# Kernel optimization log

Measured on AMD Instinct MI355X. Metric: run time of the kernel, lower is better.

Reference implementation:

```python
import jax, jax.numpy as jnp
import numpy as np

N = 100000
E = 3200000
D = 64


def setup_inputs() -> dict:
    key = jax.random.key(0)
    k1, k2, k3 = jax.random.split(key, 3)
    indices = jax.random.randint(k1, (2, E), 0, N, dtype=jnp.int64) if jax.config.jax_enable_x64 else jax.random.randint(k1, (2, E), 0, N, dtype=jnp.int32)
    values = jax.random.uniform(k2, (E,), dtype=jnp.float32)
    b = jax.random.normal(k3, (N, D), dtype=jnp.float32)
    return {"indices": indices, "values": values, "shape": N, "b": b}


def reference(indices, values, shape, b):
    # sparse COO [N,N] @ dense [N,D]:
    # out[r] = sum over edges e with row[e]==r of values[e] * b[col[e]]
    row, col = indices[0], indices[1]
    msgs = values[:, None] * b[col]            # [E, D] gather + scale
    out = jax.ops.segment_sum(msgs, row, num_segments=shape)  # [N, D] scatter-add
    return out
```

## Files before the change

### kernel.cpp

```cpp
#include <hip/hip_runtime.h>
#include <hip/hip_bf16.h>


#define D 64
#define BROWS 64
#define MAXNB 2048
#define CAP 2560
#define NM (CAP / 256)
#define SPILLCAP 8192

#define CROWS 2048
#define NCB 64
#define SCH_A 2048
#define CBLK 4352
#define NBLK_C 16
#define CAPC (CBLK * NBLK_C)

#define SCH 4096

__global__ __launch_bounds__(256) void spmm_atomic_kernel(
    const int* __restrict__ rows, const int* __restrict__ cols,
    const float* __restrict__ vals, const float* __restrict__ b,
    float* __restrict__ out, int E) {
  long long gid = (long long)blockIdx.x * blockDim.x + threadIdx.x;
  int e = (int)(gid >> 6);
  int d = (int)(gid & 63);
  if (e >= E) return;
  atomicAdd(&out[(long long)rows[e] * D + d], vals[e] * b[(long long)cols[e] * D + d]);
}

__device__ __forceinline__ unsigned bf16rne(float x) {
  unsigned u = __float_as_uint(x);
  return (u + 0x7FFFu + ((u >> 16) & 1u)) >> 16;
}
__global__ __launch_bounds__(256) void convert_kernel(
    const float4* __restrict__ src, uint2* __restrict__ dst, int n4) {
  int i = blockIdx.x * 256 + threadIdx.x;
  if (i >= n4) return;
  float4 f = src[i];
  dst[i] = make_uint2(bf16rne(f.x) | (bf16rne(f.y) << 16),
                      bf16rne(f.z) | (bf16rne(f.w) << 16));
}

__global__ __launch_bounds__(256) void coarse_scatter_kernel(
    const int* __restrict__ rows, const int* __restrict__ cols,
    const float* __restrict__ vals, int* __restrict__ gcoarse,
    uint2* __restrict__ cslab_lo, uint2* __restrict__ cslab_hi, int csplit,
    uint4* __restrict__ spill, int* __restrict__ spill_cnt, int E) {
  __shared__ uint2 stage[SCH_A];
  __shared__ unsigned char sbin[SCH_A];
  __shared__ int h[NCB];
  __shared__ int lst[NCB];
  __shared__ int gb[NCB];
  int t = threadIdx.x;
  if (t < NCB) h[t] = 0;
  __syncthreads();
  int start = blockIdx.x * SCH_A;
  int ec = E - start;
  if (ec > SCH_A) ec = SCH_A;

  int bin[8];
  int rank[8];
  unsigned key[8];
  float vv[8];
#pragma unroll
  for (int ki = 0; ki < 2; ki++) {
    int e0 = start + ki * 1024 + t * 4;
    int j0 = ki * 4;
    if (e0 + 3 < E) {
      int4 r = ((const int4*)(rows + start + ki * 1024))[t];
      int4 c = ((const int4*)(cols + start + ki * 1024))[t];
      float4 v = ((const float4*)(vals + start + ki * 1024))[t];
      int rl[4] = {r.x, r.y, r.z, r.w};
      int cl[4] = {c.x, c.y, c.z, c.w};
      float vl[4] = {v.x, v.y, v.z, v.w};
#pragma unroll
      for (int j = 0; j < 4; j++) {
        int bn = rl[j] >> 11;
        bin[j0 + j] = bn;
        rank[j0 + j] = atomicAdd(&h[bn], 1);
        key[j0 + j] = ((unsigned)(rl[j] & (CROWS - 1)) << 17) | (unsigned)cl[j];
        vv[j0 + j] = vl[j];
      }
    } else {
#pragma unroll
      for (int j = 0; j < 4; j++) {
        int e = e0 + j;
        bin[j0 + j] = -1;
        if (e < E) {
          int r = rows[e];
          int bn = r >> 11;
          bin[j0 + j] = bn;
          rank[j0 + j] = atomicAdd(&h[bn], 1);
          key[j0 + j] = ((unsigned)(r & (CROWS - 1)) << 17) | (unsigned)cols[e];
          vv[j0 + j] = vals[e];
        }
      }
    }
  }
  __syncthreads();
  if (t < NCB) {
    int c = h[t];
    int x = c;
#pragma unroll
    for (int off = 1; off < 64; off <<= 1) {
      int u = __shfl_up(x, off);
      if (t >= off) x += u;
    }
    lst[t] = x - c;
    gb[t] = c ? atomicAdd(&gcoarse[t], c) : 0;
  }
  __syncthreads();
#pragma unroll
  for (int j = 0; j < 8; j++) {
    if (bin[j] >= 0) {
      int pos = lst[bin[j]] + rank[j];
      stage[pos] = make_uint2(key[j], __float_as_uint(vv[j]));
      sbin[pos] = (unsigned char)bin[j];
    }
  }
  __syncthreads();
  for (int i = t; i < ec; i += 256) {
    int bn = sbin[i];
    uint2 p = stage[i];
    int pin = gb[bn] + (i - lst[bn]);
    if (pin < CAPC) {
      uint2* slab = (bn < csplit) ? (cslab_lo + (size_t)bn * CAPC)
                                  : (cslab_hi + (size_t)(bn - csplit) * CAPC);
      slab[pin] = p;
    } else {
      int sp = atomicAdd(spill_cnt, 1);
      if (sp < SPILLCAP)
        spill[sp] = make_uint4((unsigned)((bn << 11) | (int)(p.x >> 17)),
                               p.x & 0x1FFFFu, p.y, 0u);
    }
  }
}

__global__ __launch_bounds__(256) void fine_scatter_kernel(
    const int* __restrict__ gcoarse, const uint2* __restrict__ cslab_lo,
    const uint2* __restrict__ cslab_hi, int csplit, int* __restrict__ gcount,
    uint2* __restrict__ pairs, uint4* __restrict__ spill,
    int* __restrict__ spill_cnt) {
  int c = blockIdx.x >> 4;
  int blk = blockIdx.x & 15;
  int cnt = gcoarse[c];
  if (cnt > CAPC) cnt = CAPC;
  int base = blk * CBLK;
  int ec = cnt - base;
  if (ec <= 0) return;
  if (ec > CBLK) ec = CBLK;
  const uint2* src = ((c < csplit) ? (cslab_lo + (size_t)c * CAPC)
                                   : (cslab_hi + (size_t)(c - csplit) * CAPC)) +
                     base;
  __shared__ uint2 stage[CBLK];
  __shared__ unsigned char sbin[CBLK];
  __shared__ int h[32];
  __shared__ int lst[32];
  __shared__ int gb[32];
  int t = threadIdx.x;
  if (t < 32) h[t] = 0;
  __syncthreads();
  int rank[17];
#pragma unroll
  for (int k = 0; k < 17; k++) {
    int i = k * 256 + t;
    if (i < ec) rank[k] = atomicAdd(&h[src[i].x >> 23], 1);
  }
  __syncthreads();
  if (t < 32) {
    int cn = h[t];
    int x = cn;
#pragma unroll
    for (int off = 1; off < 32; off <<= 1) {
      int u = __shfl_up(x, off);
      if (t >= off) x += u;
    }
    lst[t] = x - cn;
    gb[t] = cn ? atomicAdd(&gcount[c * 32 + t], cn) : 0;
  }
  __syncthreads();
#pragma unroll
  for (int k = 0; k < 17; k++) {
    int i = k * 256 + t;
    if (i < ec) {
      uint2 p = src[i];
      int f = (int)(p.x >> 23);
      int pos = lst[f] + rank[k];
      unsigned key2 = (((p.x >> 17) & 63u) << 26) | ((p.x & 0x1FFFFu) << 7);
      stage[pos] = make_uint2(key2, p.y);
      sbin[pos] = (unsigned char)f;
    }
  }
  __syncthreads();
  for (int i = t; i < ec; i += 256) {
    int f = sbin[i];
    uint2 p = stage[i];
    int pin = gb[f] + (i - lst[f]);
    int gbkt = c * 32 + f;
    if (pin < CAP) {
      pairs[(size_t)gbkt * CAP + pin] = p;
    } else {
      int sp = atomicAdd(spill_cnt, 1);
      if (sp < SPILLCAP)
        spill[sp] = make_uint4((unsigned)(gbkt * 64 + (int)(p.x >> 26)),
                               (p.x >> 7) & 0x1FFFFu, p.y, 0u);
    }
  }
}

__global__ __launch_bounds__(256) void binned_scatter_kernel(
    const int* __restrict__ rows, const int* __restrict__ cols,
    const float* __restrict__ vals, int* __restrict__ gcount,
    uint2* __restrict__ pairs, uint4* __restrict__ spill,
    int* __restrict__ spill_cnt, int E, int NB) {
  __shared__ int h[MAXNB];
  __shared__ int baseoff[MAXNB];
  int t = threadIdx.x;
  for (int i = t; i < NB; i += 256) h[i] = 0;
  __syncthreads();
  int start = blockIdx.x * SCH;
  bool full = (start + SCH <= E);
  int4 r4[4];
  int rank[16];
  if (full) {
#pragma unroll
    for (int ki = 0; ki < 4; ki++) {
      r4[ki] = ((const int4*)(rows + start + ki * 1024))[t];
      rank[4 * ki + 0] = atomicAdd(&h[r4[ki].x >> 6], 1);
      rank[4 * ki + 1] = atomicAdd(&h[r4[ki].y >> 6], 1);
      rank[4 * ki + 2] = atomicAdd(&h[r4[ki].z >> 6], 1);
      rank[4 * ki + 3] = atomicAdd(&h[r4[ki].w >> 6], 1);
    }
  } else {
#pragma unroll
    for (int ki = 0; ki < 4; ki++) {
      int e = start + ki * 1024 + t * 4;
      int4 rr = make_int4(0, 0, 0, 0);
      if (e + 0 < E) { rr.x = rows[e + 0]; rank[4 * ki + 0] = atomicAdd(&h[rr.x >> 6], 1); }
      if (e + 1 < E) { rr.y = rows[e + 1]; rank[4 * ki + 1] = atomicAdd(&h[rr.y >> 6], 1); }
      if (e + 2 < E) { rr.z = rows[e + 2]; rank[4 * ki + 2] = atomicAdd(&h[rr.z >> 6], 1); }
      if (e + 3 < E) { rr.w = rows[e + 3]; rank[4 * ki + 3] = atomicAdd(&h[rr.w >> 6], 1); }
      r4[ki] = rr;
    }
  }
  __syncthreads();
  for (int i = t; i < NB; i += 256)
    baseoff[i] = h[i] ? atomicAdd(&gcount[i], h[i]) : 0;
  __syncthreads();
#pragma unroll
  for (int ki = 0; ki < 4; ki++) {
    int e = start + ki * 1024 + t * 4;
    int cc[4], rr[4] = {r4[ki].x, r4[ki].y, r4[ki].z, r4[ki].w};
    float vv[4];
    if (full) {
      int4 c4 = ((const int4*)(cols + start + ki * 1024))[t];
      float4 v4 = ((const float4*)(vals + start + ki * 1024))[t];
      cc[0] = c4.x; cc[1] = c4.y; cc[2] = c4.z; cc[3] = c4.w;
      vv[0] = v4.x; vv[1] = v4.y; vv[2] = v4.z; vv[3] = v4.w;
    } else {
#pragma unroll
      for (int j = 0; j < 4; j++) {
        cc[j] = (e + j < E) ? cols[e + j] : 0;
        vv[j] = (e + j < E) ? vals[e + j] : 0.f;
      }
    }
#pragma unroll
    for (int j = 0; j < 4; j++) {
      if (e + j < E) {
        int r = rr[j];
        int bk = r >> 6;
        int pin = baseoff[bk] + rank[4 * ki + j];
        if (pin < CAP) {
          unsigned key = ((unsigned)(r & (BROWS - 1)) << 26) |
                         ((unsigned)cc[j] << 7);
          pairs[(size_t)bk * CAP + pin] = make_uint2(key, __float_as_uint(vv[j]));
        } else {
          int sp = atomicAdd(spill_cnt, 1);
          if (sp < SPILLCAP)
            spill[sp] = make_uint4((unsigned)r, (unsigned)cc[j],
                                   __float_as_uint(vv[j]), 0u);
        }
      }
    }
  }
}

__global__ __launch_bounds__(256) void spmm_fused_kernel(
    const uint2* __restrict__ pairs, const int* __restrict__ gcount,
    const uint2* __restrict__ b16, float* __restrict__ out, int N) {
  __shared__ uint2 lp[CAP];
  __shared__ int cnt64[64];
  __shared__ int roff[65];
  int bkt = blockIdx.x;
  int cnt = gcount[bkt];
  if (cnt > CAP) cnt = CAP;
  const uint2* src = pairs + (size_t)bkt * CAP;
  int t = threadIdx.x;
  if (t < 64) cnt64[t] = 0;
  __syncthreads();
  uint2 mine[NM];
  int rk[NM];
#pragma unroll
  for (int k = 0; k < NM; k++) {
    int i = t + k * 256;
    if (i < cnt) {
      mine[k] = src[i];
      rk[k] = atomicAdd(&cnt64[mine[k].x >> 26], 1);
    }
  }
  __syncthreads();
  if (t < 64) {
    int v = cnt64[t];
    int x = v;
    for (int off = 1; off < 64; off <<= 1) {
      int u = __shfl_up(x, off);
      if (t >= off) x += u;
    }
    roff[t] = x - v;
    if (t == 63) roff[64] = x;
  }
  __syncthreads();
#pragma unroll
  for (int k = 0; k < NM; k++) {
    int i = t + k * 256;
    if (i < cnt)
      lp[roff[mine[k].x >> 26] + rk[k]] =
          make_uint2(mine[k].x & 0x03FFFF80u, mine[k].y);
  }
  __syncthreads();
  int lane = t & 63;
  int wv = t >> 6;
  int g = lane >> 3;
  int l8 = lane & 7;
  int gid32 = wv * 8 + g;
  const char* bq = (const char*)b16 + (l8 << 4);
  int row_base = bkt * BROWS;
#pragma unroll
  for (int rr = 0; rr < 2; rr++) {
    int r = gid32 + 32 * rr;
    int gr = row_base + r;
    int j0 = roff[r], j1 = roff[r + 1];
    float acc[8] = {0.f, 0.f, 0.f, 0.f, 0.f, 0.f, 0.f, 0.f};
    for (int base = j0; base < j1; base += 4) {
      uint4 bv[4];
      float vv[4];
#pragma unroll
      for (int k = 0; k < 4; k++) {
        int idx = base + k;
        int ic = (idx < j1) ? idx : j0;
        uint2 p = lp[ic];
        bv[k] = *(const uint4*)(bq + p.x);
        vv[k] = (idx < j1) ? __uint_as_float(p.y) : 0.f;
      }
#pragma unroll
      for (int k = 0; k < 4; k++) {
        unsigned u0 = bv[k].x, u1 = bv[k].y, u2 = bv[k].z, u3 = bv[k].w;
        float v = vv[k];
        acc[0] += v * __uint_as_float(u0 << 16);
        acc[1] += v * __uint_as_float(u0 & 0xFFFF0000u);
        acc[2] += v * __uint_as_float(u1 << 16);
        acc[3] += v * __uint_as_float(u1 & 0xFFFF0000u);
        acc[4] += v * __uint_as_float(u2 << 16);
        acc[5] += v * __uint_as_float(u2 & 0xFFFF0000u);
        acc[6] += v * __uint_as_float(u3 << 16);
        acc[7] += v * __uint_as_float(u3 & 0xFFFF0000u);
      }
    }
    if (gr < N) {
      float4* dst = (float4*)(out + (size_t)gr * D + l8 * 8);
      dst[0] = make_float4(acc[0], acc[1], acc[2], acc[3]);
      dst[1] = make_float4(acc[4], acc[5], acc[6], acc[7]);
    }
  }
}

__global__ __launch_bounds__(256) void spill_fix_kernel(
    const uint4* __restrict__ spill, const int* __restrict__ spill_cnt,
    const float* __restrict__ b, float* __restrict__ out) {
  int n = *spill_cnt;
  if (n > SPILLCAP) n = SPILLCAP;
  int lane = threadIdx.x & 63;
  int w = (int)((blockIdx.x * blockDim.x + threadIdx.x) >> 6);
  int nw = (int)((gridDim.x * blockDim.x) >> 6);
  for (int s = w; s < n; s += nw) {
    uint4 e = spill[s];
    atomicAdd(&out[(size_t)e.x * D + lane],
              __uint_as_float(e.z) * b[(size_t)e.y * D + lane]);
  }
}

extern "C" void kernel_launch(void* const* d_in, const int* in_sizes, int n_in,
                              void* d_out, int out_size, void* d_ws, size_t ws_size,
                              hipStream_t stream) {
  const int* indices = (const int*)d_in[0];
  const float* vals  = (const float*)d_in[1];
  const float* b     = (const float*)d_in[3];

  int E = in_sizes[1];
  int N = in_sizes[3] / D;
  const int* rows = indices;
  const int* cols = indices + E;

  int NB = (N + BROWS - 1) / BROWS;
  int NC = (N + CROWS - 1) / CROWS;
  int n4 = N * D / 4;

  size_t off_gcount  = 0;
  size_t off_gcoarse = off_gcount + (size_t)MAXNB * 4;
  size_t off_scnt    = off_gcoarse + (size_t)NCB * 4;
  size_t off_spill   = (off_scnt + 4 + 15) & ~(size_t)15;
  size_t off_pairs   = off_spill + (size_t)SPILLCAP * 16;
  size_t npbkt       = (size_t)NC * 32;
  size_t off_b16     = off_pairs + npbkt * CAP * 8;
  size_t off_cextra  = off_b16 + (size_t)N * D * 2;
  size_t outbytes    = (size_t)out_size * 4;
  int csplit = (int)(outbytes / ((size_t)CAPC * 8));
  if (csplit > NC) csplit = NC;
  size_t cextra = (size_t)(NC - csplit) * CAPC * 8;
  size_t need2 = off_cextra + cextra;

  if (ws_size >= need2 && NC <= NCB && (int)npbkt <= MAXNB && NB <= MAXNB) {
    char*  ws        = (char*)d_ws;
    int*   gcount    = (int*)(ws + off_gcount);
    int*   gcoarse   = (int*)(ws + off_gcoarse);
    int*   spill_cnt = (int*)(ws + off_scnt);
    uint4* spill     = (uint4*)(ws + off_spill);
    uint2* pairs     = (uint2*)(ws + off_pairs);
    uint2* b16       = (uint2*)(ws + off_b16);
    uint2* cslab_lo  = (uint2*)d_out;
    uint2* cslab_hi  = (uint2*)(ws + off_cextra);

    hipMemsetAsync(gcount, 0, (size_t)MAXNB * 4 + (size_t)NCB * 4 + 4, stream);
    convert_kernel<<<(n4 + 255) / 256, 256, 0, stream>>>(
        (const float4*)b, b16, n4);
    coarse_scatter_kernel<<<(E + SCH_A - 1) / SCH_A, 256, 0, stream>>>(
        rows, cols, vals, gcoarse, cslab_lo, cslab_hi, csplit,
        spill, spill_cnt, E);
    fine_scatter_kernel<<<NC * NBLK_C, 256, 0, stream>>>(
        gcoarse, cslab_lo, cslab_hi, csplit, gcount, pairs, spill, spill_cnt);
    spmm_fused_kernel<<<NB, 256, 0, stream>>>(pairs, gcount, b16,
                                              (float*)d_out, N);
    spill_fix_kernel<<<16, 256, 0, stream>>>(spill, spill_cnt, b,
                                             (float*)d_out);
    return;
  }

  size_t l_gcount = 0;
  size_t l_scnt   = l_gcount + (size_t)NB * 4;
  size_t l_spill  = (l_scnt + 4 + 15) & ~(size_t)15;
  size_t l_pairs  = (l_spill + (size_t)SPILLCAP * 16 + 15) & ~(size_t)15;
  size_t l_b16    = l_pairs + (size_t)NB * CAP * 8;
  size_t need1    = l_b16 + (size_t)N * D * 2;

  if (ws_size < need1 || NB > MAXNB) {
    hipMemsetAsync(d_out, 0, (size_t)out_size * sizeof(float), stream);
    long long total = (long long)E * 64;
    spmm_atomic_kernel<<<(int)((total + 255) / 256), 256, 0, stream>>>(
        rows, cols, vals, b, (float*)d_out, E);
    return;
  }

  char*  ws        = (char*)d_ws;
  int*   gcount    = (int*)(ws + l_gcount);
  int*   spill_cnt = (int*)(ws + l_scnt);
  uint4* spill     = (uint4*)(ws + l_spill);
  uint2* pairs     = (uint2*)(ws + l_pairs);
  uint2* b16       = (uint2*)(ws + l_b16);

  hipMemsetAsync(gcount, 0, (size_t)NB * 4 + 4, stream);
  convert_kernel<<<(n4 + 255) / 256, 256, 0, stream>>>(
      (const float4*)b, b16, n4);
  int scat_blocks = (E + SCH - 1) / SCH;
  binned_scatter_kernel<<<scat_blocks, 256, 0, stream>>>(
      rows, cols, vals, gcount, pairs, spill, spill_cnt, E, NB);
  spmm_fused_kernel<<<NB, 256, 0, stream>>>(pairs, gcount, b16,
                                            (float*)d_out, N);
  spill_fix_kernel<<<16, 256, 0, stream>>>(spill, spill_cnt, b, (float*)d_out);
}
```

Baseline: 247.5 us.

## Sort bucket edges by row and column chunk to localize gathers across threads

```diff
diff --git a/kernel.cpp b/kernel.cpp
--- a/kernel.cpp
+++ b/kernel.cpp
@@ -8,6 +8,8 @@
 #define CAP 2560
 #define NM (CAP / 256)
 #define SPILLCAP 8192
+#define NCHUNK 8
+#define NBINS (BROWS * NCHUNK)
 
 #define CROWS 2048
 #define NCB 64
@@ -290,87 +292,106 @@
     const uint2* __restrict__ pairs, const int* __restrict__ gcount,
     const uint2* __restrict__ b16, float* __restrict__ out, int N) {
   __shared__ uint2 lp[CAP];
-  __shared__ int cnt64[64];
-  __shared__ int roff[65];
+  __shared__ int cnt[NBINS];
+  __shared__ int roff[NBINS + 1];
+  __shared__ int wpart[4];
   int bkt = blockIdx.x;
-  int cnt = gcount[bkt];
-  if (cnt > CAP) cnt = CAP;
+  int cntE = gcount[bkt];
+  if (cntE > CAP) cntE = CAP;
   const uint2* src = pairs + (size_t)bkt * CAP;
   int t = threadIdx.x;
-  if (t < 64) cnt64[t] = 0;
+  int lane = t & 63;
+  int wv = t >> 6;
+  for (int i = t; i < NBINS; i += 256) cnt[i] = 0;
   __syncthreads();
   uint2 mine[NM];
   int rk[NM];
 #pragma unroll
   for (int k = 0; k < NM; k++) {
     int i = t + k * 256;
-    if (i < cnt) {
+    if (i < cntE) {
       mine[k] = src[i];
-      rk[k] = atomicAdd(&cnt64[mine[k].x >> 26], 1);
-    }
-  }
-  __syncthreads();
-  if (t < 64) {
-    int v = cnt64[t];
-    int x = v;
+      int bin = ((mine[k].x >> 26) << 3) | ((mine[k].x >> 21) & 7);
+      rk[k] = atomicAdd(&cnt[bin], 1);
+    }
+  }
+  __syncthreads();
+  {
+    int c0 = cnt[2 * t];
+    int c1 = cnt[2 * t + 1];
+    int s = c0 + c1;
+    int x = s;
+#pragma unroll
     for (int off = 1; off < 64; off <<= 1) {
       int u = __shfl_up(x, off);
-      if (t >= off) x += u;
-    }
-    roff[t] = x - v;
-    if (t == 63) roff[64] = x;
+      if (lane >= off) x += u;
+    }
+    if (lane == 63) wpart[wv] = x;
+    __syncthreads();
+    int wbase = 0;
+    for (int w = 0; w < wv; w++) wbase += wpart[w];
+    int thoff = wbase + x - s;
+    roff[2 * t] = thoff;
+    roff[2 * t + 1] = thoff + c0;
+    if (t == 255) roff[NBINS] = wbase + x;
   }
   __syncthreads();
 #pragma unroll
   for (int k = 0; k < NM; k++) {
     int i = t + k * 256;
-    if (i < cnt)
-      lp[roff[mine[k].x >> 26] + rk[k]] =
-          make_uint2(mine[k].x & 0x03FFFF80u, mine[k].y);
-  }
-  __syncthreads();
-  int lane = t & 63;
-  int wv = t >> 6;
+    if (i < cntE) {
+      int bin = ((mine[k].x >> 26) << 3) | ((mine[k].x >> 21) & 7);
+      lp[roff[bin] + rk[k]] = make_uint2(mine[k].x & 0x03FFFF80u, mine[k].y);
+    }
+  }
+  __syncthreads();
   int g = lane >> 3;
   int l8 = lane & 7;
   int gid32 = wv * 8 + g;
   const char* bq = (const char*)b16 + (l8 << 4);
   int row_base = bkt * BROWS;
+  float acc[2][8] = {{0.f, 0.f, 0.f, 0.f, 0.f, 0.f, 0.f, 0.f},
+                     {0.f, 0.f, 0.f, 0.f, 0.f, 0.f, 0.f, 0.f}};
+  for (int ch = 0; ch < NCHUNK; ch++) {
+#pragma unroll
+    for (int rr = 0; rr < 2; rr++) {
+      int r = gid32 + 32 * rr;
+      int bin = (r << 3) | ch;
+      int j0 = roff[bin], j1 = roff[bin + 1];
+      for (int base = j0; base < j1; base += 4) {
+        uint4 bv[4];
+        float vv[4];
+#pragma unroll
+        for (int k = 0; k < 4; k++) {
+          int idx = base + k;
+          int ic = (idx < j1) ? idx : j0;
+          uint2 p = lp[ic];
+          bv[k] = *(const uint4*)(bq + p.x);
+          vv[k] = (idx < j1) ? __uint_as_float(p.y) : 0.f;
+        }
+#pragma unroll
+        for (int k = 0; k < 4; k++) {
+          unsigned u0 = bv[k].x, u1 = bv[k].y, u2 = bv[k].z, u3 = bv[k].w;
+          float v = vv[k];
+          acc[rr][0] += v * __uint_as_float(u0 << 16);
+          acc[rr][1] += v * __uint_as_float(u0 & 0xFFFF0000u);
+          acc[rr][2] += v * __uint_as_float(u1 << 16);
+          acc[rr][3] += v * __uint_as_float(u1 & 0xFFFF0000u);
+          acc[rr][4] += v * __uint_as_float(u2 << 16);
+          acc[rr][5] += v * __uint_as_float(u2 & 0xFFFF0000u);
+          acc[rr][6] += v * __uint_as_float(u3 << 16);
+          acc[rr][7] += v * __uint_as_float(u3 & 0xFFFF0000u);
+        }
+      }
+    }
+  }
 #pragma unroll
   for (int rr = 0; rr < 2; rr++) {
-    int r = gid32 + 32 * rr;
-    int gr = row_base + r;
-    int j0 = roff[r], j1 = roff[r + 1];
-    float acc[8] = {0.f, 0.f, 0.f, 0.f, 0.f, 0.f, 0.f, 0.f};
-    for (int base = j0; base < j1; base += 4) {
-      uint4 bv[4];
-      float vv[4];
-#pragma unroll
-      for (int k = 0; k < 4; k++) {
-        int idx = base + k;
-        int ic = (idx < j1) ? idx : j0;
-        uint2 p = lp[ic];
-        bv[k] = *(const uint4*)(bq + p.x);
-        vv[k] = (idx < j1) ? __uint_as_float(p.y) : 0.f;
-      }
-#pragma unroll
-      for (int k = 0; k < 4; k++) {
-        unsigned u0 = bv[k].x, u1 = bv[k].y, u2 = bv[k].z, u3 = bv[k].w;
-        float v = vv[k];
-        acc[0] += v * __uint_as_float(u0 << 16);
-        acc[1] += v * __uint_as_float(u0 & 0xFFFF0000u);
-        acc[2] += v * __uint_as_float(u1 << 16);
-        acc[3] += v * __uint_as_float(u1 & 0xFFFF0000u);
-        acc[4] += v * __uint_as_float(u2 << 16);
-        acc[5] += v * __uint_as_float(u2 & 0xFFFF0000u);
-        acc[6] += v * __uint_as_float(u3 << 16);
-        acc[7] += v * __uint_as_float(u3 & 0xFFFF0000u);
-      }
-    }
+    int gr = row_base + gid32 + 32 * rr;
     if (gr < N) {
       float4* dst = (float4*)(out + (size_t)gr * D + l8 * 8);
-      dst[0] = make_float4(acc[0], acc[1], acc[2], acc[3]);
-      dst[1] = make_float4(acc[4], acc[5], acc[6], acc[7]);
+      dst[0] = make_float4(acc[rr][0], acc[rr][1], acc[rr][2], acc[rr][3]);
+      dst[1] = make_float4(acc[rr][4], acc[rr][5], acc[rr][6], acc[rr][7]);
     }
   }
 }
```

After: 228.9 us. 7.5% less time.
